# Kernel optimization log

Measured on AMD Instinct MI355X. Metric: run time of the kernel, lower is better.

## Reference

```python
import jax, jax.numpy as jnp
import numpy as np


def setup_inputs() -> dict:
    key = jax.random.key(0)
    k1, k2 = jax.random.split(key)
    N, C, H, W = 8, 3, 512, 1024
    img = jax.random.normal(k1, (N, C, H, W), dtype=jnp.float32)
    flo = jax.random.normal(k2, (N, 2, H, W), dtype=jnp.float32)
    return {"img": img, "flo": flo}


def _splat(img_nhwc, ix, iy, w, H, W):
    # img_nhwc: (N,H,W,C); ix,iy: int32 (N,H,W) absolute target coords; w: (N,H,W)
    N = img_nhwc.shape[0]
    C = img_nhwc.shape[-1]
    valid = (ix >= 0) & (ix < H) & (iy >= 0) & (iy < W)
    w = jnp.where(valid, w, 0.0)
    ixc = jnp.clip(ix, 0, H - 1)
    iyc = jnp.clip(iy, 0, W - 1)
    n_idx = jnp.arange(N, dtype=jnp.int32)[:, None, None]
    tid = (n_idx * H + ixc) * W + iyc            # (N,H,W) flat index into N*H*W
    tid = tid.reshape(-1)
    vals = (img_nhwc * w[..., None]).reshape(-1, C)
    imgw = jnp.zeros((N * H * W, C), dtype=img_nhwc.dtype).at[tid].add(vals)
    onew = jnp.zeros((N * H * W,), dtype=img_nhwc.dtype).at[tid].add(w.reshape(-1))
    imgw = imgw.reshape(N, H, W, C).transpose(0, 3, 1, 2)          # (N,C,H,W)
    onew = jnp.broadcast_to(onew.reshape(N, 1, H, W), (N, C, H, W))
    return imgw, onew


def _forward(img, flo):
    N, C, H, W = img.shape
    y = flo[:, 0]                                # (N,H,W) row offset
    x = flo[:, 1]                                # (N,H,W) col offset
    x1 = jnp.floor(x); x2 = x1 + 1.0
    y1 = jnp.floor(y); y2 = y1 + 1.0
    # gaussian splat weights
    dx1 = (x - x1) ** 2; dx2 = (x - x2) ** 2
    dy1 = (y - y1) ** 2; dy2 = (y - y2) ** 2
    w11 = jnp.exp(-(dx1 + dy1)); w12 = jnp.exp(-(dx1 + dy2))
    w21 = jnp.exp(-(dx2 + dy1)); w22 = jnp.exp(-(dx2 + dy2))
    # base grid + integer shift -> absolute target coords
    bx = jnp.arange(H, dtype=jnp.int32)[None, :, None]   # row index
    by = jnp.arange(W, dtype=jnp.int32)[None, None, :]   # col index
    img_nhwc = img.transpose(0, 2, 3, 1)
    out = []
    for sx, sy, w in ((x1, y1, w11), (x1, y2, w12), (x2, y1, w21), (x2, y2, w22)):
        ix = sx.astype(jnp.int32) + bx
        iy = sy.astype(jnp.int32) + by
        out.append(_splat(img_nhwc, ix, iy, w, H, W))
    imgw = out[0][0] + out[1][0] + out[2][0] + out[3][0]
    o = out[0][1] + out[1][1] + out[2][1] + out[3][1]
    return imgw, o


def reference(img, flo):
    return _forward(img, flo)
```

## Files before the change

kernel.cpp:

```cpp
#include <hip/hip_runtime.h>
#include <stdint.h>

constexpr int Nn = 8;
constexpr int Cc = 3;
constexpr int Hh = 512;
constexpr int Ww = 1024;
constexpr int HW = Hh * Ww;
constexpr int NCHW = Nn * Cc * HW;

constexpr int TH = 16;
constexpr int TW = 32;
constexpr int R  = 4;
constexpr int RH = TH + 2 * R;
constexpr int RW = TW + 2 * R;
constexpr int NPIX = RH * RW;
constexpr int ITERS = (NPIX + 255) / 256;
constexpr int TILE_PIX = TH * TW;
constexpr int SLOTS = 6;

typedef float fvec4 __attribute__((ext_vector_type(4)));
typedef __attribute__((address_space(3))) float lds_f;

__device__ __forceinline__ void ds_fadd4(lds_f* p, float a, float b, float c, float d) {
    asm volatile(
        "ds_add_f32 %0, %1\n\t"
        "ds_add_f32 %0, %2 offset:2048\n\t"
        "ds_add_f32 %0, %3 offset:4096\n\t"
        "ds_add_f32 %0, %4 offset:6144"
        :: "v"(p), "v"(a), "v"(b), "v"(c), "v"(d) : "memory");
}

__global__ __launch_bounds__(256, 2) void splat_tiled(
        const float* __restrict__ img,
        const float* __restrict__ flo,
        float* __restrict__ out,
        unsigned int* __restrict__ cnt,
        unsigned int* __restrict__ list,
        unsigned int cap) {
    __shared__ unsigned int s_cnt[TILE_PIX];
    __shared__ float s_slot0[TILE_PIX * SLOTS];
    __shared__ float s_slot1[TILE_PIX * SLOTS];
    __shared__ float s_slot2[TILE_PIX * SLOTS];
    __shared__ float s_slot3[TILE_PIX * SLOTS];
    __shared__ float s_ovf[4 * TILE_PIX];
    const int tid = threadIdx.x;
    #pragma unroll
    for (int i = tid; i < TILE_PIX; i += 256) s_cnt[i] = 0u;
    #pragma unroll
    for (int i = tid; i < 4 * TILE_PIX; i += 256) s_ovf[i] = 0.0f;
    __syncthreads();

    const int tw0 = blockIdx.x * TW;
    const int th0 = blockIdx.y * TH;
    const int n   = blockIdx.z;
    const float* __restrict__ floy = flo + (size_t)(n * 2 + 0) * HW;
    const float* __restrict__ flox = flo + (size_t)(n * 2 + 1) * HW;
    const float* __restrict__ imgn = img + (size_t)n * Cc * HW;

    float sy[ITERS], sx[ITERS], u0[ITERS], u1[ITERS], u2[ITERS];
    #pragma unroll
    for (int it = 0; it < ITERS; ++it) {
        int i  = tid + 256 * it;
        int ic = i < NPIX ? i : NPIX - 1;
        int rh = ic / RW;
        int rw = ic - rh * RW;
        int h  = th0 - R + rh;
        int w  = tw0 - R + rw;
        int hc = h < 0 ? 0 : (h > Hh - 1 ? Hh - 1 : h);
        int wc = w < 0 ? 0 : (w > Ww - 1 ? Ww - 1 : w);
        int hwc = hc * Ww + wc;
        sy[it] = floy[hwc];
        sx[it] = flox[hwc];
        u0[it] = imgn[hwc];
        u1[it] = imgn[HW + hwc];
        u2[it] = imgn[2 * HW + hwc];
    }

    #pragma unroll
    for (int it = 0; it < ITERS; ++it) {
        int i  = tid + 256 * it;
        int rh = i / RW;
        int rw = i - rh * RW;
        int h  = th0 - R + rh;
        int w  = tw0 - R + rw;
        bool live = (i < NPIX) & (h >= 0) & (h < Hh) & (w >= 0) & (w < Ww);

        float y = sy[it], x = sx[it];
        float x1f = floorf(x), y1f = floorf(y);
        float fx = x - x1f, fy = y - y1f;
        float gx1 = fx * fx, gx2 = (fx - 1.0f) * (fx - 1.0f);
        float gy1 = fy * fy, gy2 = (fy - 1.0f) * (fy - 1.0f);
        float w11 = __expf(-(gx1 + gy1));
        float w12 = __expf(-(gx1 + gy2));
        float w21 = __expf(-(gx2 + gy1));
        float w22 = __expf(-(gx2 + gy2));

        int ox = (int)x1f, oy = (int)y1f;
        bool okh1 = (ox >= -R)     & (ox <= R);
        bool okh2 = (ox + 1 >= -R) & (ox + 1 <= R);
        bool okw1 = (oy >= -R)     & (oy <= R);
        bool okw2 = (oy + 1 >= -R) & (oy + 1 <= R);

        int lh1 = ox + rh - R;
        int lh2 = lh1 + 1;
        int lw1 = oy + rw - R;
        int lw2 = lw1 + 1;

        float i0 = u0[it], i1 = u1[it], i2 = u2[it];

        auto corner = [&](int lh, int lw, bool okc, float wt) {
            bool ok = live & okc &
                      ((unsigned)lh < (unsigned)TH) & ((unsigned)lw < (unsigned)TW);
            if (ok) {
                int pix = lh * TW + lw;
                unsigned int idx = atomicAdd(&s_cnt[pix], 1u);
                if (idx < (unsigned)SLOTS) {
                    int sb = pix * SLOTS + (int)idx;
                    s_slot0[sb] = i0 * wt;
                    s_slot1[sb] = i1 * wt;
                    s_slot2[sb] = i2 * wt;
                    s_slot3[sb] = wt;
                } else {
                    ds_fadd4((lds_f*)s_ovf + pix, i0 * wt, i1 * wt, i2 * wt, wt);
                }
            }
        };
        corner(lh1, lw1, okh1 & okw1, w11);
        corner(lh1, lw2, okh1 & okw2, w12);
        corner(lh2, lw1, okh2 & okw1, w21);
        corner(lh2, lw2, okh2 & okw2, w22);

        bool owned = ((unsigned)(rh - R) < (unsigned)TH) &
                     ((unsigned)(rw - R) < (unsigned)TW);
        bool outl = owned & ((x >= (float)R) | (x < -(float)R) |
                             (y >= (float)R) | (y < -(float)R));
        if (__builtin_expect(outl, 0)) {
            if (cnt != nullptr) {
                unsigned int id = atomicAdd(cnt, 1u);
                if (id < cap) list[id] = (unsigned int)(n * HW + (h * Ww + w));
            }
        }
    }
    __syncthreads();

    float* __restrict__ imgw  = out;
    float* __restrict__ o_out = out + NCHW;
    const size_t nb = (size_t)n * Cc * HW;
    #pragma unroll
    for (int itr = 0; itr < 2; ++itr) {
        int pix = tid + 256 * itr;
        unsigned int k = s_cnt[pix];
        if (k > (unsigned)SLOTS) k = SLOTS;
        float s0 = s_ovf[pix];
        float s1 = s_ovf[TILE_PIX + pix];
        float s2 = s_ovf[2 * TILE_PIX + pix];
        float s3 = s_ovf[3 * TILE_PIX + pix];
        int base = pix * SLOTS;
        #pragma unroll
        for (int j = 0; j < SLOTS; ++j) {
            if ((unsigned)j < k) {
                s0 += s_slot0[base + j];
                s1 += s_slot1[base + j];
                s2 += s_slot2[base + j];
                s3 += s_slot3[base + j];
            }
        }
        int lh = pix >> 5, lw = pix & 31;
        size_t hw = (size_t)(th0 + lh) * Ww + (tw0 + lw);
        __builtin_nontemporal_store(s0, imgw + nb + hw);
        __builtin_nontemporal_store(s1, imgw + nb + HW + hw);
        __builtin_nontemporal_store(s2, imgw + nb + 2 * HW + hw);
        __builtin_nontemporal_store(s3, o_out + nb + hw);
        __builtin_nontemporal_store(s3, o_out + nb + HW + hw);
        __builtin_nontemporal_store(s3, o_out + nb + 2 * HW + hw);
    }
}

__global__ void zero_cnt(unsigned int* __restrict__ cnt) {
    if (threadIdx.x == 0 && blockIdx.x == 0) *cnt = 0u;
}

__device__ __forceinline__ void apply_outlier_px(
        const float* __restrict__ img, float* __restrict__ imgw,
        float* __restrict__ o_out, int n, int hw, float y, float x) {
    int h = hw >> 10;
    int w = hw & (Ww - 1);
    float x1f = floorf(x), y1f = floorf(y);
    float fx = x - x1f, fy = y - y1f;
    float gx1 = fx * fx, gx2 = (fx - 1.0f) * (fx - 1.0f);
    float gy1 = fy * fy, gy2 = (fy - 1.0f) * (fy - 1.0f);
    float wts[4] = { __expf(-(gx1 + gy1)), __expf(-(gx1 + gy2)),
                     __expf(-(gx2 + gy1)), __expf(-(gx2 + gy2)) };
    int bx = (int)x1f, by = (int)y1f;
    int oh[4] = { bx, bx, bx + 1, bx + 1 };
    int ow[4] = { by, by + 1, by, by + 1 };
    float i0 = img[(size_t)(n * Cc + 0) * HW + hw];
    float i1 = img[(size_t)(n * Cc + 1) * HW + hw];
    float i2 = img[(size_t)(n * Cc + 2) * HW + hw];
    const size_t nb = (size_t)n * Cc * HW;
    #pragma unroll
    for (int c = 0; c < 4; ++c) {
        if (oh[c] >= -R && oh[c] <= R && ow[c] >= -R && ow[c] <= R) continue;
        int ix = h + oh[c];
        int iy = w + ow[c];
        if (ix < 0 || ix >= Hh || iy < 0 || iy >= Ww) continue;
        int t = ix * Ww + iy;
        float wt = wts[c];
        atomicAdd(&imgw[nb + t], i0 * wt);
        atomicAdd(&imgw[nb + HW + t], i1 * wt);
        atomicAdd(&imgw[nb + 2 * HW + t], i2 * wt);
        atomicAdd(&o_out[nb + t], wt);
        atomicAdd(&o_out[nb + HW + t], wt);
        atomicAdd(&o_out[nb + 2 * HW + t], wt);
    }
}

__global__ __launch_bounds__(256) void fixup(
        const float* __restrict__ img,
        const float* __restrict__ flo,
        float* __restrict__ out,
        const unsigned int* __restrict__ cnt,
        const unsigned int* __restrict__ list,
        unsigned int cap) {
    float* imgw  = out;
    float* o_out = out + NCHW;
    unsigned int total = *cnt;
    unsigned int gid = blockIdx.x * blockDim.x + threadIdx.x;
    unsigned int stride = gridDim.x * blockDim.x;
    if (total <= cap) {
        for (unsigned int j = gid; j < total; j += stride) {
            int idx = (int)list[j];
            int n  = idx / HW;
            int hw = idx - n * HW;
            float y = flo[(size_t)(n * 2 + 0) * HW + hw];
            float x = flo[(size_t)(n * 2 + 1) * HW + hw];
            apply_outlier_px(img, imgw, o_out, n, hw, y, x);
        }
    } else {
        for (unsigned int j = gid; j < (unsigned)(Nn * HW / 4); j += stride) {
            int n   = j / (HW / 4);
            int q   = j - n * (HW / 4);
            int hw0 = q * 4;
            const fvec4 y4 = *(const fvec4*)&flo[(size_t)(n * 2 + 0) * HW + hw0];
            const fvec4 x4 = *(const fvec4*)&flo[(size_t)(n * 2 + 1) * HW + hw0];
            #pragma unroll
            for (int k = 0; k < 4; ++k) {
                float x = x4[k], y = y4[k];
                if (x < (float)R && x >= -(float)R && y < (float)R && y >= -(float)R) continue;
                apply_outlier_px(img, imgw, o_out, n, hw0 + k, y, x);
            }
        }
    }
}

__global__ __launch_bounds__(256) void rescan_all(
        const float* __restrict__ img,
        const float* __restrict__ flo,
        float* __restrict__ out) {
    float* imgw  = out;
    float* o_out = out + NCHW;
    unsigned int gid = blockIdx.x * blockDim.x + threadIdx.x;
    unsigned int stride = gridDim.x * blockDim.x;
    for (unsigned int j = gid; j < (unsigned)(Nn * HW / 4); j += stride) {
        int n   = j / (HW / 4);
        int q   = j - n * (HW / 4);
        int hw0 = q * 4;
        const fvec4 y4 = *(const fvec4*)&flo[(size_t)(n * 2 + 0) * HW + hw0];
        const fvec4 x4 = *(const fvec4*)&flo[(size_t)(n * 2 + 1) * HW + hw0];
        #pragma unroll
        for (int k = 0; k < 4; ++k) {
            float x = x4[k], y = y4[k];
            if (x < (float)R && x >= -(float)R && y < (float)R && y >= -(float)R) continue;
            apply_outlier_px(img, imgw, o_out, n, hw0 + k, y, x);
        }
    }
}

extern "C" void kernel_launch(void* const* d_in, const int* in_sizes, int n_in,
                              void* d_out, int out_size, void* d_ws, size_t ws_size,
                              hipStream_t stream) {
    const float* img = (const float*)d_in[0];
    const float* flo = (const float*)d_in[1];
    float* out = (float*)d_out;

    dim3 block(256);
    dim3 grid(Ww / TW, Hh / TH, Nn);

    bool have_ws = (d_ws != nullptr) && (ws_size >= 64);
    if (have_ws) {
        unsigned int* cnt  = (unsigned int*)d_ws;
        unsigned int* list = cnt + 1;
        size_t cap_sz = (ws_size - sizeof(unsigned int)) / sizeof(unsigned int);
        unsigned int cap = cap_sz > 0x3FFFFFu ? 0x3FFFFFu : (unsigned int)cap_sz;
        zero_cnt<<<1, 64, 0, stream>>>(cnt);
        splat_tiled<<<grid, block, 0, stream>>>(img, flo, out, cnt, list, cap);
        fixup<<<64, 256, 0, stream>>>(img, flo, out, cnt, list, cap);
    } else {
        splat_tiled<<<grid, block, 0, stream>>>(img, flo, out, nullptr, nullptr, 0u);
        rescan_all<<<512, 256, 0, stream>>>(img, flo, out);
    }
}
```

Measured before the change: 228.3 us.

## Record one anchor entry per source pixel and compute corner weights at gather time

Each source pixel now appends a single record (three image values plus fractional offsets) to a per-anchor LDS slot list, instead of four weighted records, one per target corner. The gather phase reads the four neighbouring anchors and evaluates the exp weights there. This cuts LDS atomics and scatter writes by about four times, in exchange for more exp work and more LDS reads in the gather. The outlier path now uses a full-grid rescan kernel with one thread per four pixels, replacing the workspace list, the counter-zeroing kernel and the fixup kernel. That removes a launch and the global counter atomics, but the whole flow field is now always read a second time.

```diff
diff --git a/kernel.cpp b/kernel.cpp
--- a/kernel.cpp
+++ b/kernel.cpp
@@ -16,7 +16,8 @@
 constexpr int NPIX = RH * RW;
 constexpr int ITERS = (NPIX + 255) / 256;
 constexpr int TILE_PIX = TH * TW;
-constexpr int SLOTS = 6;
+constexpr int NP = (TH + 1) * (TW + 1);
+constexpr int SLOTS = 5;
 
 typedef float fvec4 __attribute__((ext_vector_type(4)));
 typedef __attribute__((address_space(3))) float lds_f;
@@ -33,21 +34,18 @@
 __global__ __launch_bounds__(256, 2) void splat_tiled(
         const float* __restrict__ img,
         const float* __restrict__ flo,
-        float* __restrict__ out,
-        unsigned int* __restrict__ cnt,
-        unsigned int* __restrict__ list,
-        unsigned int cap) {
-    __shared__ unsigned int s_cnt[TILE_PIX];
-    __shared__ float s_slot0[TILE_PIX * SLOTS];
-    __shared__ float s_slot1[TILE_PIX * SLOTS];
-    __shared__ float s_slot2[TILE_PIX * SLOTS];
-    __shared__ float s_slot3[TILE_PIX * SLOTS];
+        float* __restrict__ out) {
+    __shared__ unsigned int s_cnt[NP];
+    __shared__ float s_slot[SLOTS * NP * 5];
     __shared__ float s_ovf[4 * TILE_PIX];
     const int tid = threadIdx.x;
-    #pragma unroll
-    for (int i = tid; i < TILE_PIX; i += 256) s_cnt[i] = 0u;
-    #pragma unroll
-    for (int i = tid; i < 4 * TILE_PIX; i += 256) s_ovf[i] = 0.0f;
+    for (int i = tid; i < NP; i += 256) s_cnt[i] = 0u;
+    {
+        fvec4* a4 = (fvec4*)s_ovf;
+        fvec4 z = {0.f, 0.f, 0.f, 0.f};
+        a4[tid]       = z;
+        a4[tid + 256] = z;
+    }
     __syncthreads();
 
     const int tw0 = blockIdx.x * TW;
@@ -88,56 +86,37 @@
         float y = sy[it], x = sx[it];
         float x1f = floorf(x), y1f = floorf(y);
         float fx = x - x1f, fy = y - y1f;
-        float gx1 = fx * fx, gx2 = (fx - 1.0f) * (fx - 1.0f);
-        float gy1 = fy * fy, gy2 = (fy - 1.0f) * (fy - 1.0f);
-        float w11 = __expf(-(gx1 + gy1));
-        float w12 = __expf(-(gx1 + gy2));
-        float w21 = __expf(-(gx2 + gy1));
-        float w22 = __expf(-(gx2 + gy2));
-
         int ox = (int)x1f, oy = (int)y1f;
-        bool okh1 = (ox >= -R)     & (ox <= R);
-        bool okh2 = (ox + 1 >= -R) & (ox + 1 <= R);
-        bool okw1 = (oy >= -R)     & (oy <= R);
-        bool okw2 = (oy + 1 >= -R) & (oy + 1 <= R);
-
-        int lh1 = ox + rh - R;
-        int lh2 = lh1 + 1;
-        int lw1 = oy + rw - R;
-        int lw2 = lw1 + 1;
-
-        float i0 = u0[it], i1 = u1[it], i2 = u2[it];
-
-        auto corner = [&](int lh, int lw, bool okc, float wt) {
-            bool ok = live & okc &
-                      ((unsigned)lh < (unsigned)TH) & ((unsigned)lw < (unsigned)TW);
-            if (ok) {
-                int pix = lh * TW + lw;
-                unsigned int idx = atomicAdd(&s_cnt[pix], 1u);
-                if (idx < (unsigned)SLOTS) {
-                    int sb = pix * SLOTS + (int)idx;
-                    s_slot0[sb] = i0 * wt;
-                    s_slot1[sb] = i1 * wt;
-                    s_slot2[sb] = i2 * wt;
-                    s_slot3[sb] = wt;
-                } else {
-                    ds_fadd4((lds_f*)s_ovf + pix, i0 * wt, i1 * wt, i2 * wt, wt);
+        bool patchok = (ox >= -R) & (ox <= R - 1) & (oy >= -R) & (oy <= R - 1);
+        int ah = ox + rh - R;
+        int aw = oy + rw - R;
+        bool rec = live & patchok & (ah >= -1) & (ah <= TH - 1)
+                                  & (aw >= -1) & (aw <= TW - 1);
+        if (rec) {
+            int aIdx = (ah + 1) * (TW + 1) + (aw + 1);
+            unsigned int idx = atomicAdd(&s_cnt[aIdx], 1u);
+            if (idx < (unsigned)SLOTS) {
+                float* e = &s_slot[((int)idx * NP + aIdx) * 5];
+                e[0] = u0[it];
+                e[1] = u1[it];
+                e[2] = u2[it];
+                e[3] = fx;
+                e[4] = fy;
+            } else {
+                float i0 = u0[it], i1 = u1[it], i2 = u2[it];
+                #pragma unroll
+                for (int a = 0; a < 2; ++a) {
+                    #pragma unroll
+                    for (int b = 0; b < 2; ++b) {
+                        int t_h = ah + a, t_w = aw + b;
+                        if ((unsigned)t_h < (unsigned)TH && (unsigned)t_w < (unsigned)TW) {
+                            float dx = fx - (float)a, dy = fy - (float)b;
+                            float wt = __expf(-(dx * dx + dy * dy));
+                            ds_fadd4((lds_f*)s_ovf + (t_h * TW + t_w),
+                                     i0 * wt, i1 * wt, i2 * wt, wt);
+                        }
+                    }
                 }
-            }
-        };
-        corner(lh1, lw1, okh1 & okw1, w11);
-        corner(lh1, lw2, okh1 & okw2, w12);
-        corner(lh2, lw1, okh2 & okw1, w21);
-        corner(lh2, lw2, okh2 & okw2, w22);
-
-        bool owned = ((unsigned)(rh - R) < (unsigned)TH) &
-                     ((unsigned)(rw - R) < (unsigned)TW);
-        bool outl = owned & ((x >= (float)R) | (x < -(float)R) |
-                             (y >= (float)R) | (y < -(float)R));
-        if (__builtin_expect(outl, 0)) {
-            if (cnt != nullptr) {
-                unsigned int id = atomicAdd(cnt, 1u);
-                if (id < cap) list[id] = (unsigned int)(n * HW + (h * Ww + w));
             }
         }
     }
@@ -149,23 +128,33 @@
     #pragma unroll
     for (int itr = 0; itr < 2; ++itr) {
         int pix = tid + 256 * itr;
-        unsigned int k = s_cnt[pix];
-        if (k > (unsigned)SLOTS) k = SLOTS;
+        int lh = pix >> 5, lw = pix & 31;
         float s0 = s_ovf[pix];
         float s1 = s_ovf[TILE_PIX + pix];
         float s2 = s_ovf[2 * TILE_PIX + pix];
         float s3 = s_ovf[3 * TILE_PIX + pix];
-        int base = pix * SLOTS;
         #pragma unroll
-        for (int j = 0; j < SLOTS; ++j) {
-            if ((unsigned)j < k) {
-                s0 += s_slot0[base + j];
-                s1 += s_slot1[base + j];
-                s2 += s_slot2[base + j];
-                s3 += s_slot3[base + j];
+        for (int a = 0; a < 2; ++a) {
+            #pragma unroll
+            for (int b = 0; b < 2; ++b) {
+                int aIdx = (lh - a + 1) * (TW + 1) + (lw - b + 1);
+                unsigned int k = s_cnt[aIdx];
+                if (k > (unsigned)SLOTS) k = SLOTS;
+                #pragma unroll
+                for (int j = 0; j < SLOTS; ++j) {
+                    if ((unsigned)j < k) {
+                        const float* e = &s_slot[(j * NP + aIdx) * 5];
+                        float e0 = e[0], e1 = e[1], e2 = e[2];
+                        float dx = e[3] - (float)a, dy = e[4] - (float)b;
+                        float wt = __expf(-(dx * dx + dy * dy));
+                        s0 += e0 * wt;
+                        s1 += e1 * wt;
+                        s2 += e2 * wt;
+                        s3 += wt;
+                    }
+                }
             }
         }
-        int lh = pix >> 5, lw = pix & 31;
         size_t hw = (size_t)(th0 + lh) * Ww + (tw0 + lw);
         __builtin_nontemporal_store(s0, imgw + nb + hw);
         __builtin_nontemporal_store(s1, imgw + nb + HW + hw);
@@ -176,102 +165,50 @@
     }
 }
 
-__global__ void zero_cnt(unsigned int* __restrict__ cnt) {
-    if (threadIdx.x == 0 && blockIdx.x == 0) *cnt = 0u;
-}
-
-__device__ __forceinline__ void apply_outlier_px(
-        const float* __restrict__ img, float* __restrict__ imgw,
-        float* __restrict__ o_out, int n, int hw, float y, float x) {
-    int h = hw >> 10;
-    int w = hw & (Ww - 1);
-    float x1f = floorf(x), y1f = floorf(y);
-    float fx = x - x1f, fy = y - y1f;
-    float gx1 = fx * fx, gx2 = (fx - 1.0f) * (fx - 1.0f);
-    float gy1 = fy * fy, gy2 = (fy - 1.0f) * (fy - 1.0f);
-    float wts[4] = { __expf(-(gx1 + gy1)), __expf(-(gx1 + gy2)),
-                     __expf(-(gx2 + gy1)), __expf(-(gx2 + gy2)) };
-    int bx = (int)x1f, by = (int)y1f;
-    int oh[4] = { bx, bx, bx + 1, bx + 1 };
-    int ow[4] = { by, by + 1, by, by + 1 };
-    float i0 = img[(size_t)(n * Cc + 0) * HW + hw];
-    float i1 = img[(size_t)(n * Cc + 1) * HW + hw];
-    float i2 = img[(size_t)(n * Cc + 2) * HW + hw];
-    const size_t nb = (size_t)n * Cc * HW;
-    #pragma unroll
-    for (int c = 0; c < 4; ++c) {
-        if (oh[c] >= -R && oh[c] <= R && ow[c] >= -R && ow[c] <= R) continue;
-        int ix = h + oh[c];
-        int iy = w + ow[c];
-        if (ix < 0 || ix >= Hh || iy < 0 || iy >= Ww) continue;
-        int t = ix * Ww + iy;
-        float wt = wts[c];
-        atomicAdd(&imgw[nb + t], i0 * wt);
-        atomicAdd(&imgw[nb + HW + t], i1 * wt);
-        atomicAdd(&imgw[nb + 2 * HW + t], i2 * wt);
-        atomicAdd(&o_out[nb + t], wt);
-        atomicAdd(&o_out[nb + HW + t], wt);
-        atomicAdd(&o_out[nb + 2 * HW + t], wt);
-    }
-}
-
-__global__ __launch_bounds__(256) void fixup(
-        const float* __restrict__ img,
-        const float* __restrict__ flo,
-        float* __restrict__ out,
-        const unsigned int* __restrict__ cnt,
-        const unsigned int* __restrict__ list,
-        unsigned int cap) {
-    float* imgw  = out;
-    float* o_out = out + NCHW;
-    unsigned int total = *cnt;
-    unsigned int gid = blockIdx.x * blockDim.x + threadIdx.x;
-    unsigned int stride = gridDim.x * blockDim.x;
-    if (total <= cap) {
-        for (unsigned int j = gid; j < total; j += stride) {
-            int idx = (int)list[j];
-            int n  = idx / HW;
-            int hw = idx - n * HW;
-            float y = flo[(size_t)(n * 2 + 0) * HW + hw];
-            float x = flo[(size_t)(n * 2 + 1) * HW + hw];
-            apply_outlier_px(img, imgw, o_out, n, hw, y, x);
-        }
-    } else {
-        for (unsigned int j = gid; j < (unsigned)(Nn * HW / 4); j += stride) {
-            int n   = j / (HW / 4);
-            int q   = j - n * (HW / 4);
-            int hw0 = q * 4;
-            const fvec4 y4 = *(const fvec4*)&flo[(size_t)(n * 2 + 0) * HW + hw0];
-            const fvec4 x4 = *(const fvec4*)&flo[(size_t)(n * 2 + 1) * HW + hw0];
-            #pragma unroll
-            for (int k = 0; k < 4; ++k) {
-                float x = x4[k], y = y4[k];
-                if (x < (float)R && x >= -(float)R && y < (float)R && y >= -(float)R) continue;
-                apply_outlier_px(img, imgw, o_out, n, hw0 + k, y, x);
-            }
-        }
-    }
-}
-
 __global__ __launch_bounds__(256) void rescan_all(
         const float* __restrict__ img,
         const float* __restrict__ flo,
         float* __restrict__ out) {
     float* imgw  = out;
     float* o_out = out + NCHW;
-    unsigned int gid = blockIdx.x * blockDim.x + threadIdx.x;
-    unsigned int stride = gridDim.x * blockDim.x;
-    for (unsigned int j = gid; j < (unsigned)(Nn * HW / 4); j += stride) {
-        int n   = j / (HW / 4);
-        int q   = j - n * (HW / 4);
-        int hw0 = q * 4;
-        const fvec4 y4 = *(const fvec4*)&flo[(size_t)(n * 2 + 0) * HW + hw0];
-        const fvec4 x4 = *(const fvec4*)&flo[(size_t)(n * 2 + 1) * HW + hw0];
+    unsigned int j = blockIdx.x * blockDim.x + threadIdx.x;
+    if (j >= (unsigned)(Nn * HW / 4)) return;
+    int n   = j / (HW / 4);
+    int q   = j - n * (HW / 4);
+    int hw0 = q * 4;
+    const fvec4 y4 = *(const fvec4*)&flo[(size_t)(n * 2 + 0) * HW + hw0];
+    const fvec4 x4 = *(const fvec4*)&flo[(size_t)(n * 2 + 1) * HW + hw0];
+    #pragma unroll
+    for (int k = 0; k < 4; ++k) {
+        float x = x4[k], y = y4[k];
+        if (x >= -(float)R && x < (float)R && y >= -(float)R && y < (float)R) continue;
+        int hw = hw0 + k;
+        int h = hw >> 10;
+        int w = hw & (Ww - 1);
+        float x1f = floorf(x), y1f = floorf(y);
+        float fx = x - x1f, fy = y - y1f;
+        int bx = (int)x1f, by = (int)y1f;
+        float i0 = img[(size_t)(n * Cc + 0) * HW + hw];
+        float i1 = img[(size_t)(n * Cc + 1) * HW + hw];
+        float i2 = img[(size_t)(n * Cc + 2) * HW + hw];
+        const size_t nb = (size_t)n * Cc * HW;
         #pragma unroll
-        for (int k = 0; k < 4; ++k) {
-            float x = x4[k], y = y4[k];
-            if (x < (float)R && x >= -(float)R && y < (float)R && y >= -(float)R) continue;
-            apply_outlier_px(img, imgw, o_out, n, hw0 + k, y, x);
+        for (int a = 0; a < 2; ++a) {
+            #pragma unroll
+            for (int b = 0; b < 2; ++b) {
+                int ix = h + bx + a;
+                int iy = w + by + b;
+                if (ix < 0 || ix >= Hh || iy < 0 || iy >= Ww) continue;
+                float dx = fx - (float)a, dy = fy - (float)b;
+                float wt = __expf(-(dx * dx + dy * dy));
+                int t = ix * Ww + iy;
+                atomicAdd(&imgw[nb + t], i0 * wt);
+                atomicAdd(&imgw[nb + HW + t], i1 * wt);
+                atomicAdd(&imgw[nb + 2 * HW + t], i2 * wt);
+                atomicAdd(&o_out[nb + t], wt);
+                atomicAdd(&o_out[nb + HW + t], wt);
+                atomicAdd(&o_out[nb + 2 * HW + t], wt);
+            }
         }
     }
 }
@@ -282,21 +219,10 @@
     const float* img = (const float*)d_in[0];
     const float* flo = (const float*)d_in[1];
     float* out = (float*)d_out;
+    (void)d_ws; (void)ws_size;
 
     dim3 block(256);
     dim3 grid(Ww / TW, Hh / TH, Nn);
-
-    bool have_ws = (d_ws != nullptr) && (ws_size >= 64);
-    if (have_ws) {
-        unsigned int* cnt  = (unsigned int*)d_ws;
-        unsigned int* list = cnt + 1;
-        size_t cap_sz = (ws_size - sizeof(unsigned int)) / sizeof(unsigned int);
-        unsigned int cap = cap_sz > 0x3FFFFFu ? 0x3FFFFFu : (unsigned int)cap_sz;
-        zero_cnt<<<1, 64, 0, stream>>>(cnt);
-        splat_tiled<<<grid, block, 0, stream>>>(img, flo, out, cnt, list, cap);
-        fixup<<<64, 256, 0, stream>>>(img, flo, out, cnt, list, cap);
-    } else {
-        splat_tiled<<<grid, block, 0, stream>>>(img, flo, out, nullptr, nullptr, 0u);
-        rescan_all<<<512, 256, 0, stream>>>(img, flo, out);
-    }
-}
+    splat_tiled<<<grid, block, 0, stream>>>(img, flo, out);
+    rescan_all<<<(Nn * HW / 4 + 255) / 256, 256, 0, stream>>>(img, flo, out);
+}
```

Measured after the change: 229.0 us. About the same (+0.3%).
